# Performance work log

Hardware: AMD Instinct MI355X
Metric: run time of the kernel (lower is better)

## Reference

```python
import jax, jax.numpy as jnp
import numpy as np

N_NODES = 50000
N_EDGES = 800000
D_IN = 64
D_HID = 64
D_OUT = 64


def setup_inputs() -> dict:
    key = jax.random.key(0)
    ks = jax.random.split(key, 6)
    X = jax.random.normal(ks[0], (N_NODES, D_IN), dtype=jnp.float32)
    edge_index = jax.random.randint(ks[1], (2, N_EDGES), 0, N_NODES, dtype=jnp.int64)
    edge_weight = jax.random.uniform(ks[2], (N_EDGES,), dtype=jnp.float32)
    W1 = jax.random.normal(ks[3], (D_IN, D_HID), dtype=jnp.float32) / np.float32(np.sqrt(D_IN))
    b1 = jnp.zeros((D_HID,), dtype=jnp.float32)
    W2 = jax.random.normal(ks[4], (D_HID, D_OUT), dtype=jnp.float32) / np.float32(np.sqrt(D_HID))
    b2 = jnp.zeros((D_OUT,), dtype=jnp.float32)
    return {"X": X, "edge_weight": edge_weight, "W1": W1, "b1": b1,
            "W2": W2, "b2": b2, "edge_index": edge_index}


def reference(X, edge_weight, W1, b1, W2, b2, edge_index):
    # conv(A, X) = (A @ X) @ W + b with sparse A given as (edge_index, edge_weight)
    src = edge_index[0]
    dst = edge_index[1]

    def agg(H):
        # weighted neighborhood sum: [E, d] messages scattered to [N, d]
        msgs = edge_weight[:, None] * H[src]
        return jax.ops.segment_sum(msgs, dst, num_segments=N_NODES)

    # layer 1: conv -> relu (dropout p=0 is identity)
    H = jax.nn.relu(agg(X) @ W1 + b1)
    # last layer: conv, no final activation (l_act=None)
    return agg(H) @ W2 + b2
```

## Files before the change

### kernel.cpp

```cpp
#include <hip/hip_runtime.h>

#define D 64

#define NB 256
#define RB 256

template <bool PRE>
__global__ __launch_bounds__(256, 4) void gemm64_kernel(
    const float* __restrict__ A, const float* __restrict__ W,
    const float* __restrict__ bpre, float* __restrict__ out, int N) {
  __shared__ float sA[64][68];
  __shared__ float sW[64][68];
  const int t = threadIdx.x;
  const int rowBase = blockIdx.x * 64;

#pragma unroll
  for (int i = t * 4; i < 4096; i += 1024) {
    const int k = i >> 6, c = i & 63;
    *reinterpret_cast<float4*>(&sW[k][c]) =
        *reinterpret_cast<const float4*>(W + i);
  }
#pragma unroll
  for (int i = t * 4; i < 4096; i += 1024) {
    const int r = i >> 6, k = i & 63;
    const int row = rowBase + r;
    float4 a = make_float4(0.f, 0.f, 0.f, 0.f);
    if (row < N) a = *reinterpret_cast<const float4*>(A + (size_t)row * D + k);
    if (PRE) {
      const float4 b = *reinterpret_cast<const float4*>(bpre + k);
      a.x = fmaxf(a.x + b.x, 0.f);
      a.y = fmaxf(a.y + b.y, 0.f);
      a.z = fmaxf(a.z + b.z, 0.f);
      a.w = fmaxf(a.w + b.w, 0.f);
    }
    *reinterpret_cast<float4*>(&sA[r][k]) = a;
  }
  __syncthreads();

  const int ty = t >> 4, tx = t & 15;
  float4 acc0 = make_float4(0.f, 0.f, 0.f, 0.f);
  float4 acc1 = make_float4(0.f, 0.f, 0.f, 0.f);
  float4 acc2 = make_float4(0.f, 0.f, 0.f, 0.f);
  float4 acc3 = make_float4(0.f, 0.f, 0.f, 0.f);

#pragma unroll 4
  for (int kq = 0; kq < 16; ++kq) {
    const float4 w0 = *reinterpret_cast<const float4*>(&sW[kq * 4 + 0][tx * 4]);
    const float4 w1 = *reinterpret_cast<const float4*>(&sW[kq * 4 + 1][tx * 4]);
    const float4 w2 = *reinterpret_cast<const float4*>(&sW[kq * 4 + 2][tx * 4]);
    const float4 w3 = *reinterpret_cast<const float4*>(&sW[kq * 4 + 3][tx * 4]);
    const float4 a0 = *reinterpret_cast<const float4*>(&sA[ty * 4 + 0][kq * 4]);
    const float4 a1 = *reinterpret_cast<const float4*>(&sA[ty * 4 + 1][kq * 4]);
    const float4 a2 = *reinterpret_cast<const float4*>(&sA[ty * 4 + 2][kq * 4]);
    const float4 a3 = *reinterpret_cast<const float4*>(&sA[ty * 4 + 3][kq * 4]);
#define FMA4(ACC, AV)                                                     \
    ACC.x += AV.x * w0.x + AV.y * w1.x + AV.z * w2.x + AV.w * w3.x;       \
    ACC.y += AV.x * w0.y + AV.y * w1.y + AV.z * w2.y + AV.w * w3.y;       \
    ACC.z += AV.x * w0.z + AV.y * w1.z + AV.z * w2.z + AV.w * w3.z;       \
    ACC.w += AV.x * w0.w + AV.y * w1.w + AV.z * w2.w + AV.w * w3.w;
    FMA4(acc0, a0) FMA4(acc1, a1) FMA4(acc2, a2) FMA4(acc3, a3)
#undef FMA4
  }

  const int row0 = rowBase + ty * 4;
  if (row0 + 0 < N) *reinterpret_cast<float4*>(out + (size_t)(row0 + 0) * D + tx * 4) = acc0;
  if (row0 + 1 < N) *reinterpret_cast<float4*>(out + (size_t)(row0 + 1) * D + tx * 4) = acc1;
  if (row0 + 2 < N) *reinterpret_cast<float4*>(out + (size_t)(row0 + 2) * D + tx * 4) = acc2;
  if (row0 + 3 < N) *reinterpret_cast<float4*>(out + (size_t)(row0 + 3) * D + tx * 4) = acc3;
}

__global__ __launch_bounds__(256, 4) void hist_gemm_kernel(
    const int* __restrict__ dst, int* __restrict__ countsB, int E, int epb,
    const float* __restrict__ A, const float* __restrict__ W,
    float* __restrict__ out, int N) {
  __shared__ float sA[64][68];
  __shared__ float sW[64][68];
  const int t = threadIdx.x;

  if ((int)blockIdx.x < NB) {
    int* h = reinterpret_cast<int*>(&sA[0][0]);
    h[t] = 0;
    __syncthreads();
    const int base = blockIdx.x * epb;
    const int lim = min(base + epb, E);
    for (int i = base + t; i < lim; i += 256) atomicAdd(&h[dst[i] >> 8], 1);
    __syncthreads();
    countsB[blockIdx.x * RB + t] = h[t];
    return;
  }

  const int rowBase = ((int)blockIdx.x - NB) * 64;
#pragma unroll
  for (int i = t * 4; i < 4096; i += 1024) {
    const int k = i >> 6, c = i & 63;
    *reinterpret_cast<float4*>(&sW[k][c]) =
        *reinterpret_cast<const float4*>(W + i);
  }
#pragma unroll
  for (int i = t * 4; i < 4096; i += 1024) {
    const int r = i >> 6, k = i & 63;
    const int row = rowBase + r;
    float4 a = make_float4(0.f, 0.f, 0.f, 0.f);
    if (row < N) a = *reinterpret_cast<const float4*>(A + (size_t)row * D + k);
    *reinterpret_cast<float4*>(&sA[r][k]) = a;
  }
  __syncthreads();

  const int ty = t >> 4, tx = t & 15;
  float4 acc0 = make_float4(0.f, 0.f, 0.f, 0.f);
  float4 acc1 = make_float4(0.f, 0.f, 0.f, 0.f);
  float4 acc2 = make_float4(0.f, 0.f, 0.f, 0.f);
  float4 acc3 = make_float4(0.f, 0.f, 0.f, 0.f);

#pragma unroll 4
  for (int kq = 0; kq < 16; ++kq) {
    const float4 w0 = *reinterpret_cast<const float4*>(&sW[kq * 4 + 0][tx * 4]);
    const float4 w1 = *reinterpret_cast<const float4*>(&sW[kq * 4 + 1][tx * 4]);
    const float4 w2 = *reinterpret_cast<const float4*>(&sW[kq * 4 + 2][tx * 4]);
    const float4 w3 = *reinterpret_cast<const float4*>(&sW[kq * 4 + 3][tx * 4]);
    const float4 a0 = *reinterpret_cast<const float4*>(&sA[ty * 4 + 0][kq * 4]);
    const float4 a1 = *reinterpret_cast<const float4*>(&sA[ty * 4 + 1][kq * 4]);
    const float4 a2 = *reinterpret_cast<const float4*>(&sA[ty * 4 + 2][kq * 4]);
    const float4 a3 = *reinterpret_cast<const float4*>(&sA[ty * 4 + 3][kq * 4]);
#define FMA4(ACC, AV)                                                     \
    ACC.x += AV.x * w0.x + AV.y * w1.x + AV.z * w2.x + AV.w * w3.x;       \
    ACC.y += AV.x * w0.y + AV.y * w1.y + AV.z * w2.y + AV.w * w3.y;       \
    ACC.z += AV.x * w0.z + AV.y * w1.z + AV.z * w2.z + AV.w * w3.z;       \
    ACC.w += AV.x * w0.w + AV.y * w1.w + AV.z * w2.w + AV.w * w3.w;
    FMA4(acc0, a0) FMA4(acc1, a1) FMA4(acc2, a2) FMA4(acc3, a3)
#undef FMA4
  }

  const int row0 = rowBase + ty * 4;
  if (row0 + 0 < N) *reinterpret_cast<float4*>(out + (size_t)(row0 + 0) * D + tx * 4) = acc0;
  if (row0 + 1 < N) *reinterpret_cast<float4*>(out + (size_t)(row0 + 1) * D + tx * 4) = acc1;
  if (row0 + 2 < N) *reinterpret_cast<float4*>(out + (size_t)(row0 + 2) * D + tx * 4) = acc2;
  if (row0 + 3 < N) *reinterpret_cast<float4*>(out + (size_t)(row0 + 3) * D + tx * 4) = acc3;
}

__global__ __launch_bounds__(256) void p1_scatter_kernel(
    const int* __restrict__ src, const int* __restrict__ dst,
    const float* __restrict__ ew, const int* __restrict__ countsB,
    int* __restrict__ binBaseG, int2* __restrict__ tmp, int E, int epb) {
  __shared__ int s[RB];
  __shared__ int cur[RB];
  const int t = threadIdx.x;
  const int b = blockIdx.x;

  int total = 0, pre = 0;
#pragma unroll 8
  for (int i = 0; i < NB; ++i) {
    const int c = countsB[i * RB + t];
    if (i == b) pre = total;
    total += c;
  }
  s[t] = total;
  __syncthreads();
  for (int off = 1; off < 256; off <<= 1) {
    int x = (t >= off) ? s[t - off] : 0;
    __syncthreads();
    s[t] += x;
    __syncthreads();
  }
  const int binBase = s[t] - total;
  cur[t] = binBase + pre;
  if (b == 0) {
    binBaseG[t] = binBase;
    if (t == 255) binBaseG[256] = s[255];
  }
  __syncthreads();

  const int base = b * epb;
  const int lim = min(base + epb, E);
  for (int i = base + t; i < lim; i += 256) {
    const int d = dst[i];
    const unsigned sv = (unsigned)src[i];
    const float w = ew[i];
    const int pos = atomicAdd(&cur[d >> 8], 1);
    tmp[pos] = make_int2((int)((unsigned)d | (sv << 16)), __float_as_int(w));
  }
}

__global__ __launch_bounds__(256) void p2_kernel(
    const int2* __restrict__ tmp, const int* __restrict__ binBaseG,
    int* __restrict__ offs, int2* __restrict__ pairs, int N) {
  __shared__ int h[RB];
  __shared__ int s[RB];
  __shared__ int cur[RB];
  const int t = threadIdx.x;
  const int b = blockIdx.x;
  const int segBeg = binBaseG[b];
  const int segEnd = binBaseG[b + 1];

  h[t] = 0;
  __syncthreads();
  for (int i = segBeg + t; i < segEnd; i += 256)
    atomicAdd(&h[tmp[i].x & 255], 1);
  __syncthreads();

  const int v = h[t];
  s[t] = v;
  __syncthreads();
  for (int off = 1; off < 256; off <<= 1) {
    int x = (t >= off) ? s[t - off] : 0;
    __syncthreads();
    s[t] += x;
    __syncthreads();
  }
  const int excl = s[t] - v;
  cur[t] = segBeg + excl;
  const int node = b * RB + t;
  if (node <= N) offs[node] = segBeg + excl;
  __syncthreads();

  for (int i = segBeg + t; i < segEnd; i += 256) {
    const int2 r = tmp[i];
    const int lo = r.x & 255;
    const int pos = atomicAdd(&cur[lo], 1);
    pairs[pos] = make_int2((int)(((unsigned)r.x) >> 16), r.y);
  }
}

__global__ __launch_bounds__(256) void hist_kernel(
    const int* __restrict__ dst, int* __restrict__ deg,
    int* __restrict__ posw, int E) {
  int e = blockIdx.x * 256 + threadIdx.x;
  if (e < E) posw[e] = atomicAdd(&deg[dst[e]], 1);
}

#define SCAN_CHUNK 1024
__global__ __launch_bounds__(256) void scan_part_kernel(
    const int* __restrict__ deg, int* __restrict__ offs,
    int* __restrict__ bsums, int N) {
  __shared__ int s[256];
  const int t = threadIdx.x;
  const int base = blockIdx.x * SCAN_CHUNK + t * 4;
  int v0 = 0, v1 = 0, v2 = 0, v3 = 0;
  if (base + 3 < N) {
    const int4 v = *reinterpret_cast<const int4*>(deg + base);
    v0 = v.x; v1 = v.y; v2 = v.z; v3 = v.w;
  } else {
    if (base + 0 < N) v0 = deg[base + 0];
    if (base + 1 < N) v1 = deg[base + 1];
    if (base + 2 < N) v2 = deg[base + 2];
  }
  const int tsum = v0 + v1 + v2 + v3;
  s[t] = tsum;
  __syncthreads();
  for (int off = 1; off < 256; off <<= 1) {
    int x = (t >= off) ? s[t - off] : 0;
    __syncthreads();
    s[t] += x;
    __syncthreads();
  }
  const int excl = s[t] - tsum;
  if (base + 0 < N) offs[base + 0] = excl;
  if (base + 1 < N) offs[base + 1] = excl + v0;
  if (base + 2 < N) offs[base + 2] = excl + v0 + v1;
  if (base + 3 < N) offs[base + 3] = excl + v0 + v1 + v2;
  if (t == 255) bsums[blockIdx.x] = s[255];
}

__global__ __launch_bounds__(1024) void scan_sums_kernel(
    int* __restrict__ bsums, int* __restrict__ offsN, int nb) {
  __shared__ int s[1024];
  const int t = threadIdx.x;
  const int v = (t < nb) ? bsums[t] : 0;
  s[t] = v;
  __syncthreads();
  for (int off = 1; off < 1024; off <<= 1) {
    int x = (t >= off) ? s[t - off] : 0;
    __syncthreads();
    s[t] += x;
    __syncthreads();
  }
  if (t < nb) bsums[t] = s[t] - v;
  if (t == nb - 1) *offsN = s[t];
}

__global__ __launch_bounds__(256) void scan_add_kernel(
    int* __restrict__ offs, const int* __restrict__ bsums, int N) {
  const int i = blockIdx.x * 256 + threadIdx.x;
  if (i < N) offs[i] += bsums[i >> 10];
}

__global__ __launch_bounds__(256) void bucket_kernel(
    const int* __restrict__ src, const int* __restrict__ dst,
    const float* __restrict__ ew, const int* __restrict__ offs,
    const int* __restrict__ posw, int2* __restrict__ pairs, int E) {
  int e = blockIdx.x * 256 + threadIdx.x;
  if (e < E) {
    const int pos = offs[dst[e]] + posw[e];
    pairs[pos] = make_int2(src[e], __float_as_int(ew[e]));
  }
}

__global__ __launch_bounds__(256, 4) void agg_gemm_kernel(
    const float* __restrict__ H, const int* __restrict__ offs,
    const int2* __restrict__ pairs, const float* __restrict__ b1,
    const float* __restrict__ W, float* __restrict__ out, int N) {
  __shared__ float sA[64][68];
  __shared__ float sW[64][68];
  const int t = threadIdx.x;
  const int rowBase = blockIdx.x * 64;

#pragma unroll
  for (int i = t * 4; i < 4096; i += 1024) {
    const int k = i >> 6, c = i & 63;
    *reinterpret_cast<float4*>(&sW[k][c]) =
        *reinterpret_cast<const float4*>(W + i);
  }

  const int l4 = t & 15;
  const int sub = t >> 4;
  const float4 bb = *reinterpret_cast<const float4*>(b1 + l4 * 4);
#pragma unroll
  for (int p = 0; p < 4; ++p) {
    const int r = p * 16 + sub;
    const int node = rowBase + r;
    float4 A0 = make_float4(0.f, 0.f, 0.f, 0.f);
    float4 A1 = make_float4(0.f, 0.f, 0.f, 0.f);
    float4 A2 = make_float4(0.f, 0.f, 0.f, 0.f);
    float4 A3 = make_float4(0.f, 0.f, 0.f, 0.f);
    if (node < N) {
      const int beg = offs[node], end = offs[node + 1];
      int i = beg;
      for (; i + 4 <= end; i += 4) {
        const int2 p0 = pairs[i], p1 = pairs[i + 1], p2 = pairs[i + 2], p3 = pairs[i + 3];
        const float4 v0 = *reinterpret_cast<const float4*>(H + (size_t)p0.x * D + l4 * 4);
        const float4 v1 = *reinterpret_cast<const float4*>(H + (size_t)p1.x * D + l4 * 4);
        const float4 v2 = *reinterpret_cast<const float4*>(H + (size_t)p2.x * D + l4 * 4);
        const float4 v3 = *reinterpret_cast<const float4*>(H + (size_t)p3.x * D + l4 * 4);
        const float w0 = __int_as_float(p0.y), w1 = __int_as_float(p1.y);
        const float w2 = __int_as_float(p2.y), w3 = __int_as_float(p3.y);
        A0.x += w0 * v0.x; A0.y += w0 * v0.y; A0.z += w0 * v0.z; A0.w += w0 * v0.w;
        A1.x += w1 * v1.x; A1.y += w1 * v1.y; A1.z += w1 * v1.z; A1.w += w1 * v1.w;
        A2.x += w2 * v2.x; A2.y += w2 * v2.y; A2.z += w2 * v2.z; A2.w += w2 * v2.w;
        A3.x += w3 * v3.x; A3.y += w3 * v3.y; A3.z += w3 * v3.z; A3.w += w3 * v3.w;
      }
      for (; i < end; ++i) {
        const int2 pp = pairs[i];
        const float4 v = *reinterpret_cast<const float4*>(H + (size_t)pp.x * D + l4 * 4);
        const float w = __int_as_float(pp.y);
        A0.x += w * v.x; A0.y += w * v.y; A0.z += w * v.z; A0.w += w * v.w;
      }
    }
    float4 rr;
    rr.x = fmaxf((A0.x + A1.x) + (A2.x + A3.x) + bb.x, 0.f);
    rr.y = fmaxf((A0.y + A1.y) + (A2.y + A3.y) + bb.y, 0.f);
    rr.z = fmaxf((A0.z + A1.z) + (A2.z + A3.z) + bb.z, 0.f);
    rr.w = fmaxf((A0.w + A1.w) + (A2.w + A3.w) + bb.w, 0.f);
    *reinterpret_cast<float4*>(&sA[r][l4 * 4]) = rr;
  }
  __syncthreads();

  const int ty = t >> 4, tx = t & 15;
  float4 acc0 = make_float4(0.f, 0.f, 0.f, 0.f);
  float4 acc1 = make_float4(0.f, 0.f, 0.f, 0.f);
  float4 acc2 = make_float4(0.f, 0.f, 0.f, 0.f);
  float4 acc3 = make_float4(0.f, 0.f, 0.f, 0.f);

#pragma unroll 4
  for (int kq = 0; kq < 16; ++kq) {
    const float4 w0 = *reinterpret_cast<const float4*>(&sW[kq * 4 + 0][tx * 4]);
    const float4 w1 = *reinterpret_cast<const float4*>(&sW[kq * 4 + 1][tx * 4]);
    const float4 w2 = *reinterpret_cast<const float4*>(&sW[kq * 4 + 2][tx * 4]);
    const float4 w3 = *reinterpret_cast<const float4*>(&sW[kq * 4 + 3][tx * 4]);
    const float4 a0 = *reinterpret_cast<const float4*>(&sA[ty * 4 + 0][kq * 4]);
    const float4 a1 = *reinterpret_cast<const float4*>(&sA[ty * 4 + 1][kq * 4]);
    const float4 a2 = *reinterpret_cast<const float4*>(&sA[ty * 4 + 2][kq * 4]);
    const float4 a3 = *reinterpret_cast<const float4*>(&sA[ty * 4 + 3][kq * 4]);
#define FMA4(ACC, AV)                                                     \
    ACC.x += AV.x * w0.x + AV.y * w1.x + AV.z * w2.x + AV.w * w3.x;       \
    ACC.y += AV.x * w0.y + AV.y * w1.y + AV.z * w2.y + AV.w * w3.y;       \
    ACC.z += AV.x * w0.z + AV.y * w1.z + AV.z * w2.z + AV.w * w3.z;       \
    ACC.w += AV.x * w0.w + AV.y * w1.w + AV.z * w2.w + AV.w * w3.w;
    FMA4(acc0, a0) FMA4(acc1, a1) FMA4(acc2, a2) FMA4(acc3, a3)
#undef FMA4
  }

  const int row0 = rowBase + ty * 4;
  if (row0 + 0 < N) *reinterpret_cast<float4*>(out + (size_t)(row0 + 0) * D + tx * 4) = acc0;
  if (row0 + 1 < N) *reinterpret_cast<float4*>(out + (size_t)(row0 + 1) * D + tx * 4) = acc1;
  if (row0 + 2 < N) *reinterpret_cast<float4*>(out + (size_t)(row0 + 2) * D + tx * 4) = acc2;
  if (row0 + 3 < N) *reinterpret_cast<float4*>(out + (size_t)(row0 + 3) * D + tx * 4) = acc3;
}

template <bool BIAS>
__global__ __launch_bounds__(256) void gather_agg_kernel(
    const float* __restrict__ H, const int* __restrict__ offs,
    const int2* __restrict__ pairs,
    const float* __restrict__ bias, float* __restrict__ out, int N) {
  const int l4 = threadIdx.x & 15;
  const int node = blockIdx.x * 16 + (threadIdx.x >> 4);
  if (node >= N) return;
  const int beg = offs[node], end = offs[node + 1];
  float4 A0 = make_float4(0.f, 0.f, 0.f, 0.f);
  float4 A1 = make_float4(0.f, 0.f, 0.f, 0.f);
  float4 A2 = make_float4(0.f, 0.f, 0.f, 0.f);
  float4 A3 = make_float4(0.f, 0.f, 0.f, 0.f);
  int i = beg;
  for (; i + 4 <= end; i += 4) {
    const int2 p0 = pairs[i], p1 = pairs[i + 1], p2 = pairs[i + 2], p3 = pairs[i + 3];
    const float4 v0 = *reinterpret_cast<const float4*>(H + (size_t)p0.x * D + l4 * 4);
    const float4 v1 = *reinterpret_cast<const float4*>(H + (size_t)p1.x * D + l4 * 4);
    const float4 v2 = *reinterpret_cast<const float4*>(H + (size_t)p2.x * D + l4 * 4);
    const float4 v3 = *reinterpret_cast<const float4*>(H + (size_t)p3.x * D + l4 * 4);
    const float w0 = __int_as_float(p0.y), w1 = __int_as_float(p1.y);
    const float w2 = __int_as_float(p2.y), w3 = __int_as_float(p3.y);
    A0.x += w0 * v0.x; A0.y += w0 * v0.y; A0.z += w0 * v0.z; A0.w += w0 * v0.w;
    A1.x += w1 * v1.x; A1.y += w1 * v1.y; A1.z += w1 * v1.z; A1.w += w1 * v1.w;
    A2.x += w2 * v2.x; A2.y += w2 * v2.y; A2.z += w2 * v2.z; A2.w += w2 * v2.w;
    A3.x += w3 * v3.x; A3.y += w3 * v3.y; A3.z += w3 * v3.z; A3.w += w3 * v3.w;
  }
  for (; i < end; ++i) {
    const int2 p = pairs[i];
    const float4 v = *reinterpret_cast<const float4*>(H + (size_t)p.x * D + l4 * 4);
    const float w = __int_as_float(p.y);
    A0.x += w * v.x; A0.y += w * v.y; A0.z += w * v.z; A0.w += w * v.w;
  }
  float4 r;
  r.x = (A0.x + A1.x) + (A2.x + A3.x);
  r.y = (A0.y + A1.y) + (A2.y + A3.y);
  r.z = (A0.z + A1.z) + (A2.z + A3.z);
  r.w = (A0.w + A1.w) + (A2.w + A3.w);
  if (BIAS) {
    const float4 b = *reinterpret_cast<const float4*>(bias + l4 * 4);
    r.x += b.x; r.y += b.y; r.z += b.z; r.w += b.w;
  }
  *reinterpret_cast<float4*>(out + (size_t)node * D + l4 * 4) = r;
}

__global__ __launch_bounds__(256) void scatter_kernel(
    const float* __restrict__ H, const float* __restrict__ ew,
    const int* __restrict__ src, const int* __restrict__ dst,
    float* __restrict__ out, int nEdges) {
  const int tid = blockIdx.x * 256 + threadIdx.x;
  const int e = tid >> 4;
  if (e >= nEdges) return;
  const int c = (tid & 15) * 4;
  const float w = ew[e];
  const float4 v = *reinterpret_cast<const float4*>(H + (size_t)src[e] * D + c);
  float* o = out + (size_t)dst[e] * D + c;
  atomicAdd(o + 0, w * v.x);
  atomicAdd(o + 1, w * v.y);
  atomicAdd(o + 2, w * v.z);
  atomicAdd(o + 3, w * v.w);
}

__global__ __launch_bounds__(256) void fill_bias_kernel(
    float* __restrict__ out, const float* __restrict__ b, int total) {
  int i = blockIdx.x * 256 + threadIdx.x;
  if (i < total) out[i] = b[i & 63];
}

extern "C" void kernel_launch(void* const* d_in, const int* in_sizes, int n_in,
                              void* d_out, int out_size, void* d_ws,
                              size_t ws_size, hipStream_t stream) {
  const float* X  = (const float*)d_in[0];
  const float* ew = (const float*)d_in[1];
  const float* W1 = (const float*)d_in[2];
  const float* b1 = (const float*)d_in[3];
  const float* W2 = (const float*)d_in[4];
  const float* b2 = (const float*)d_in[5];
  const int*   ei = (const int*)d_in[6];

  const int N = in_sizes[0] / D;
  const int E = in_sizes[6] / 2;
  const int* src = ei;
  const int* dst = ei + E;
  float* out = (float*)d_out;

  char* ws = (char*)d_ws;
  float* buf0 = (float*)ws;                 ws += (size_t)N * D * 4;
  float* buf1 = (float*)ws;                 ws += (size_t)N * D * 4;
  const size_t baseBytes = (size_t)(ws - (char*)d_ws);
  int2*  pairs    = (int2*)ws;              ws += (size_t)E * 8;
  int*   offs     = (int*)ws;               ws += (size_t)(N + 1) * 4;
  int*   countsB  = (int*)ws;               ws += (size_t)NB * RB * 4;
  int*   binBaseG = (int*)ws;               ws += (size_t)(RB + 1) * 4;
  const size_t needBytes = (size_t)(ws - (char*)d_ws);

  const int gemmBlocks = (N + 63) / 64;
  const int aggBlocks  = (N + 15) / 16;
  const int edgeBlocks = (E + 255) / 256;

  if (ws_size >= needBytes) {
    if (N <= NB * RB && (size_t)N * D * 4 >= (size_t)E * 8) {
      int2* tmp = (int2*)buf1;
      const int epb = (E + NB - 1) / NB;
      hist_gemm_kernel<<<NB + gemmBlocks, 256, 0, stream>>>(
          dst, countsB, E, epb, X, W1, buf0, N);
      p1_scatter_kernel<<<NB, 256, 0, stream>>>(src, dst, ew, countsB,
                                                binBaseG, tmp, E, epb);
      p2_kernel<<<RB, 256, 0, stream>>>(tmp, binBaseG, offs, pairs, N);
    } else {
      int* deg   = (int*)buf0;
      int* bsums = (int*)buf0 + N;
      int* posw  = (int*)buf1;
      const int nb = (N + SCAN_CHUNK - 1) / SCAN_CHUNK;
      hipMemsetAsync(deg, 0, (size_t)N * 4, stream);
      hist_kernel<<<edgeBlocks, 256, 0, stream>>>(dst, deg, posw, E);
      scan_part_kernel<<<nb, 256, 0, stream>>>(deg, offs, bsums, N);
      scan_sums_kernel<<<1, 1024, 0, stream>>>(bsums, offs + N, nb);
      scan_add_kernel<<<(N + 255) / 256, 256, 0, stream>>>(offs, bsums, N);
      bucket_kernel<<<edgeBlocks, 256, 0, stream>>>(src, dst, ew, offs, posw, pairs, E);
      gemm64_kernel<false><<<gemmBlocks, 256, 0, stream>>>(X, W1, nullptr, buf0, N);
    }

    agg_gemm_kernel<<<gemmBlocks, 256, 0, stream>>>(buf0, offs, pairs, b1, W2, buf1, N);
    gather_agg_kernel<true><<<aggBlocks, 256, 0, stream>>>(buf1, offs, pairs, b2, out, N);
  } else if (ws_size >= baseBytes) {
    const int scatBlocks = (E * 16 + 255) / 256;
    const int fillBlocks = (N * D + 255) / 256;
    gemm64_kernel<false><<<gemmBlocks, 256, 0, stream>>>(X, W1, nullptr, buf0, N);
    hipMemsetAsync(buf1, 0, (size_t)N * D * 4, stream);
    scatter_kernel<<<scatBlocks, 256, 0, stream>>>(buf0, ew, src, dst, buf1, E);
    gemm64_kernel<true><<<gemmBlocks, 256, 0, stream>>>(buf1, W2, b1, buf0, N);
    fill_bias_kernel<<<fillBlocks, 256, 0, stream>>>(out, b2, N * D);
    scatter_kernel<<<scatBlocks, 256, 0, stream>>>(buf0, ew, src, dst, out, E);
  }
}
```

Measured before the change: 116.3 us.

## Use whole-wave per-node gathers and register-cached ranks in bucket sort pass

The aggregation kernels now give each node a full 64-lane wave: four groups of 16 lanes split that node's edges and are combined with xor shuffles, replacing the old scheme of one 16-lane group per node. This shortens the serial per-node edge loop and raises memory-level parallelism. The second sort pass now keeps records and their atomic ranks in registers, up to 20 per thread, and spills overflow ranks to a new global buffer, so it no longer re-reads tmp and runs a second atomic pass. The cost is more registers, shuffle work, and lanes left idle on low-degree nodes.

```diff
diff --git a/kernel.cpp b/kernel.cpp
--- a/kernel.cpp
+++ b/kernel.cpp
@@ -4,6 +4,52 @@
 
 #define NB 256
 #define RB 256
+#define P2CAP 20
+
+__device__ inline float4 f4zero() { return make_float4(0.f, 0.f, 0.f, 0.f); }
+
+__device__ inline float4 xor_add(float4 a, int m) {
+  a.x += __shfl_xor(a.x, m);
+  a.y += __shfl_xor(a.y, m);
+  a.z += __shfl_xor(a.z, m);
+  a.w += __shfl_xor(a.w, m);
+  return a;
+}
+
+__device__ inline float4 gather_rows(
+    const float* __restrict__ H, const int2* __restrict__ pairs,
+    int beg, int end, int g, int c4) {
+  float4 a0 = f4zero(), a1 = f4zero(), a2 = f4zero(), a3 = f4zero();
+  int i = beg + g;
+  for (; i + 12 < end; i += 16) {
+    const int2 p0 = pairs[i];
+    const int2 p1 = pairs[i + 4];
+    const int2 p2 = pairs[i + 8];
+    const int2 p3 = pairs[i + 12];
+    const float4 v0 = *reinterpret_cast<const float4*>(H + (size_t)p0.x * D + c4 * 4);
+    const float4 v1 = *reinterpret_cast<const float4*>(H + (size_t)p1.x * D + c4 * 4);
+    const float4 v2 = *reinterpret_cast<const float4*>(H + (size_t)p2.x * D + c4 * 4);
+    const float4 v3 = *reinterpret_cast<const float4*>(H + (size_t)p3.x * D + c4 * 4);
+    const float w0 = __int_as_float(p0.y), w1 = __int_as_float(p1.y);
+    const float w2 = __int_as_float(p2.y), w3 = __int_as_float(p3.y);
+    a0.x += w0 * v0.x; a0.y += w0 * v0.y; a0.z += w0 * v0.z; a0.w += w0 * v0.w;
+    a1.x += w1 * v1.x; a1.y += w1 * v1.y; a1.z += w1 * v1.z; a1.w += w1 * v1.w;
+    a2.x += w2 * v2.x; a2.y += w2 * v2.y; a2.z += w2 * v2.z; a2.w += w2 * v2.w;
+    a3.x += w3 * v3.x; a3.y += w3 * v3.y; a3.z += w3 * v3.z; a3.w += w3 * v3.w;
+  }
+  for (; i < end; i += 4) {
+    const int2 p = pairs[i];
+    const float4 v = *reinterpret_cast<const float4*>(H + (size_t)p.x * D + c4 * 4);
+    const float w = __int_as_float(p.y);
+    a0.x += w * v.x; a0.y += w * v.y; a0.z += w * v.z; a0.w += w * v.w;
+  }
+  float4 a;
+  a.x = (a0.x + a1.x) + (a2.x + a3.x);
+  a.y = (a0.y + a1.y) + (a2.y + a3.y);
+  a.z = (a0.z + a1.z) + (a2.z + a3.z);
+  a.w = (a0.w + a1.w) + (a2.w + a3.w);
+  return a;
+}
 
 template <bool PRE>
 __global__ __launch_bounds__(256, 4) void gemm64_kernel(
@@ -24,7 +70,7 @@
   for (int i = t * 4; i < 4096; i += 1024) {
     const int r = i >> 6, k = i & 63;
     const int row = rowBase + r;
-    float4 a = make_float4(0.f, 0.f, 0.f, 0.f);
+    float4 a = f4zero();
     if (row < N) a = *reinterpret_cast<const float4*>(A + (size_t)row * D + k);
     if (PRE) {
       const float4 b = *reinterpret_cast<const float4*>(bpre + k);
@@ -38,10 +84,7 @@
   __syncthreads();
 
   const int ty = t >> 4, tx = t & 15;
-  float4 acc0 = make_float4(0.f, 0.f, 0.f, 0.f);
-  float4 acc1 = make_float4(0.f, 0.f, 0.f, 0.f);
-  float4 acc2 = make_float4(0.f, 0.f, 0.f, 0.f);
-  float4 acc3 = make_float4(0.f, 0.f, 0.f, 0.f);
+  float4 acc0 = f4zero(), acc1 = f4zero(), acc2 = f4zero(), acc3 = f4zero();
 
 #pragma unroll 4
   for (int kq = 0; kq < 16; ++kq) {
@@ -100,17 +143,14 @@
   for (int i = t * 4; i < 4096; i += 1024) {
     const int r = i >> 6, k = i & 63;
     const int row = rowBase + r;
-    float4 a = make_float4(0.f, 0.f, 0.f, 0.f);
+    float4 a = f4zero();
     if (row < N) a = *reinterpret_cast<const float4*>(A + (size_t)row * D + k);
     *reinterpret_cast<float4*>(&sA[r][k]) = a;
   }
   __syncthreads();
 
   const int ty = t >> 4, tx = t & 15;
-  float4 acc0 = make_float4(0.f, 0.f, 0.f, 0.f);
-  float4 acc1 = make_float4(0.f, 0.f, 0.f, 0.f);
-  float4 acc2 = make_float4(0.f, 0.f, 0.f, 0.f);
-  float4 acc3 = make_float4(0.f, 0.f, 0.f, 0.f);
+  float4 acc0 = f4zero(), acc1 = f4zero(), acc2 = f4zero(), acc3 = f4zero();
 
 #pragma unroll 4
   for (int kq = 0; kq < 16; ++kq) {
@@ -183,19 +223,33 @@
 
 __global__ __launch_bounds__(256) void p2_kernel(
     const int2* __restrict__ tmp, const int* __restrict__ binBaseG,
+    int* __restrict__ rankG,
     int* __restrict__ offs, int2* __restrict__ pairs, int N) {
   __shared__ int h[RB];
   __shared__ int s[RB];
-  __shared__ int cur[RB];
   const int t = threadIdx.x;
   const int b = blockIdx.x;
   const int segBeg = binBaseG[b];
   const int segEnd = binBaseG[b + 1];
+  const int segLen = segEnd - segBeg;
 
   h[t] = 0;
   __syncthreads();
-  for (int i = segBeg + t; i < segEnd; i += 256)
-    atomicAdd(&h[tmp[i].x & 255], 1);
+
+  const int cnt = (segLen - t + 255) >> 8;
+  int2 rec[P2CAP];
+  int  rk[P2CAP];
+#pragma unroll
+  for (int k = 0; k < P2CAP; ++k) {
+    if (k < cnt) {
+      const int i = segBeg + t + (k << 8);
+      const int2 r = tmp[i];
+      rec[k] = r;
+      rk[k] = atomicAdd(&h[r.x & 255], 1);
+    }
+  }
+  for (int i = segBeg + (P2CAP << 8) + t; i < segEnd; i += 256)
+    rankG[i] = atomicAdd(&h[tmp[i].x & 255], 1);
   __syncthreads();
 
   const int v = h[t];
@@ -208,16 +262,24 @@
     __syncthreads();
   }
   const int excl = s[t] - v;
-  cur[t] = segBeg + excl;
   const int node = b * RB + t;
   if (node <= N) offs[node] = segBeg + excl;
   __syncthreads();
-
-  for (int i = segBeg + t; i < segEnd; i += 256) {
+  h[t] = segBeg + excl;
+  __syncthreads();
+
+#pragma unroll
+  for (int k = 0; k < P2CAP; ++k) {
+    if (k < cnt) {
+      const int2 r = rec[k];
+      pairs[h[r.x & 255] + rk[k]] =
+          make_int2((int)(((unsigned)r.x) >> 16), r.y);
+    }
+  }
+  for (int i = segBeg + (P2CAP << 8) + t; i < segEnd; i += 256) {
     const int2 r = tmp[i];
-    const int lo = r.x & 255;
-    const int pos = atomicAdd(&cur[lo], 1);
-    pairs[pos] = make_int2((int)(((unsigned)r.x) >> 16), r.y);
+    pairs[h[r.x & 255] + rankG[i]] =
+        make_int2((int)(((unsigned)r.x) >> 16), r.y);
   }
 }
 
@@ -311,54 +373,35 @@
         *reinterpret_cast<const float4*>(W + i);
   }
 
-  const int l4 = t & 15;
-  const int sub = t >> 4;
-  const float4 bb = *reinterpret_cast<const float4*>(b1 + l4 * 4);
-#pragma unroll
-  for (int p = 0; p < 4; ++p) {
-    const int r = p * 16 + sub;
+  const int wv = t >> 6;
+  const int lane = t & 63;
+  const int g = lane >> 4;
+  const int c4 = lane & 15;
+  const float4 bb = *reinterpret_cast<const float4*>(b1 + c4 * 4);
+
+  for (int sidx = 0; sidx < 16; ++sidx) {
+    const int r = wv * 16 + sidx;
     const int node = rowBase + r;
-    float4 A0 = make_float4(0.f, 0.f, 0.f, 0.f);
-    float4 A1 = make_float4(0.f, 0.f, 0.f, 0.f);
-    float4 A2 = make_float4(0.f, 0.f, 0.f, 0.f);
-    float4 A3 = make_float4(0.f, 0.f, 0.f, 0.f);
+    float4 a = f4zero();
     if (node < N) {
       const int beg = offs[node], end = offs[node + 1];
-      int i = beg;
-      for (; i + 4 <= end; i += 4) {
-        const int2 p0 = pairs[i], p1 = pairs[i + 1], p2 = pairs[i + 2], p3 = pairs[i + 3];
-        const float4 v0 = *reinterpret_cast<const float4*>(H + (size_t)p0.x * D + l4 * 4);
-        const float4 v1 = *reinterpret_cast<const float4*>(H + (size_t)p1.x * D + l4 * 4);
-        const float4 v2 = *reinterpret_cast<const float4*>(H + (size_t)p2.x * D + l4 * 4);
-        const float4 v3 = *reinterpret_cast<const float4*>(H + (size_t)p3.x * D + l4 * 4);
-        const float w0 = __int_as_float(p0.y), w1 = __int_as_float(p1.y);
-        const float w2 = __int_as_float(p2.y), w3 = __int_as_float(p3.y);
-        A0.x += w0 * v0.x; A0.y += w0 * v0.y; A0.z += w0 * v0.z; A0.w += w0 * v0.w;
-        A1.x += w1 * v1.x; A1.y += w1 * v1.y; A1.z += w1 * v1.z; A1.w += w1 * v1.w;
-        A2.x += w2 * v2.x; A2.y += w2 * v2.y; A2.z += w2 * v2.z; A2.w += w2 * v2.w;
-        A3.x += w3 * v3.x; A3.y += w3 * v3.y; A3.z += w3 * v3.z; A3.w += w3 * v3.w;
-      }
-      for (; i < end; ++i) {
-        const int2 pp = pairs[i];
-        const float4 v = *reinterpret_cast<const float4*>(H + (size_t)pp.x * D + l4 * 4);
-        const float w = __int_as_float(pp.y);
-        A0.x += w * v.x; A0.y += w * v.y; A0.z += w * v.z; A0.w += w * v.w;
-      }
-    }
-    float4 rr;
-    rr.x = fmaxf((A0.x + A1.x) + (A2.x + A3.x) + bb.x, 0.f);
-    rr.y = fmaxf((A0.y + A1.y) + (A2.y + A3.y) + bb.y, 0.f);
-    rr.z = fmaxf((A0.z + A1.z) + (A2.z + A3.z) + bb.z, 0.f);
-    rr.w = fmaxf((A0.w + A1.w) + (A2.w + A3.w) + bb.w, 0.f);
-    *reinterpret_cast<float4*>(&sA[r][l4 * 4]) = rr;
+      a = gather_rows(H, pairs, beg, end, g, c4);
+    }
+    a = xor_add(a, 16);
+    a = xor_add(a, 32);
+    if (g == 0) {
+      float4 rr;
+      rr.x = fmaxf(a.x + bb.x, 0.f);
+      rr.y = fmaxf(a.y + bb.y, 0.f);
+      rr.z = fmaxf(a.z + bb.z, 0.f);
+      rr.w = fmaxf(a.w + bb.w, 0.f);
+      *reinterpret_cast<float4*>(&sA[r][c4 * 4]) = rr;
+    }
   }
   __syncthreads();
 
   const int ty = t >> 4, tx = t & 15;
-  float4 acc0 = make_float4(0.f, 0.f, 0.f, 0.f);
-  float4 acc1 = make_float4(0.f, 0.f, 0.f, 0.f);
-  float4 acc2 = make_float4(0.f, 0.f, 0.f, 0.f);
-  float4 acc3 = make_float4(0.f, 0.f, 0.f, 0.f);
+  float4 acc0 = f4zero(), acc1 = f4zero(), acc2 = f4zero(), acc3 = f4zero();
 
 #pragma unroll 4
   for (int kq = 0; kq < 16; ++kq) {
@@ -387,48 +430,26 @@
 }
 
 template <bool BIAS>
-__global__ __launch_bounds__(256) void gather_agg_kernel(
+__global__ __launch_bounds__(256) void wave_agg_kernel(
     const float* __restrict__ H, const int* __restrict__ offs,
-    const int2* __restrict__ pairs,
-    const float* __restrict__ bias, float* __restrict__ out, int N) {
-  const int l4 = threadIdx.x & 15;
-  const int node = blockIdx.x * 16 + (threadIdx.x >> 4);
+    const int2* __restrict__ pairs, const float* __restrict__ bias,
+    float* __restrict__ out, int N) {
+  const int lane = threadIdx.x & 63;
+  const int g = lane >> 4;
+  const int c4 = lane & 15;
+  const int node = blockIdx.x * 4 + (threadIdx.x >> 6);
   if (node >= N) return;
   const int beg = offs[node], end = offs[node + 1];
-  float4 A0 = make_float4(0.f, 0.f, 0.f, 0.f);
-  float4 A1 = make_float4(0.f, 0.f, 0.f, 0.f);
-  float4 A2 = make_float4(0.f, 0.f, 0.f, 0.f);
-  float4 A3 = make_float4(0.f, 0.f, 0.f, 0.f);
-  int i = beg;
-  for (; i + 4 <= end; i += 4) {
-    const int2 p0 = pairs[i], p1 = pairs[i + 1], p2 = pairs[i + 2], p3 = pairs[i + 3];
-    const float4 v0 = *reinterpret_cast<const float4*>(H + (size_t)p0.x * D + l4 * 4);
-    const float4 v1 = *reinterpret_cast<const float4*>(H + (size_t)p1.x * D + l4 * 4);
-    const float4 v2 = *reinterpret_cast<const float4*>(H + (size_t)p2.x * D + l4 * 4);
-    const float4 v3 = *reinterpret_cast<const float4*>(H + (size_t)p3.x * D + l4 * 4);
-    const float w0 = __int_as_float(p0.y), w1 = __int_as_float(p1.y);
-    const float w2 = __int_as_float(p2.y), w3 = __int_as_float(p3.y);
-    A0.x += w0 * v0.x; A0.y += w0 * v0.y; A0.z += w0 * v0.z; A0.w += w0 * v0.w;
-    A1.x += w1 * v1.x; A1.y += w1 * v1.y; A1.z += w1 * v1.z; A1.w += w1 * v1.w;
-    A2.x += w2 * v2.x; A2.y += w2 * v2.y; A2.z += w2 * v2.z; A2.w += w2 * v2.w;
-    A3.x += w3 * v3.x; A3.y += w3 * v3.y; A3.z += w3 * v3.z; A3.w += w3 * v3.w;
-  }
-  for (; i < end; ++i) {
-    const int2 p = pairs[i];
-    const float4 v = *reinterpret_cast<const float4*>(H + (size_t)p.x * D + l4 * 4);
-    const float w = __int_as_float(p.y);
-    A0.x += w * v.x; A0.y += w * v.y; A0.z += w * v.z; A0.w += w * v.w;
-  }
-  float4 r;
-  r.x = (A0.x + A1.x) + (A2.x + A3.x);
-  r.y = (A0.y + A1.y) + (A2.y + A3.y);
-  r.z = (A0.z + A1.z) + (A2.z + A3.z);
-  r.w = (A0.w + A1.w) + (A2.w + A3.w);
-  if (BIAS) {
-    const float4 b = *reinterpret_cast<const float4*>(bias + l4 * 4);
-    r.x += b.x; r.y += b.y; r.z += b.z; r.w += b.w;
-  }
-  *reinterpret_cast<float4*>(out + (size_t)node * D + l4 * 4) = r;
+  float4 a = gather_rows(H, pairs, beg, end, g, c4);
+  a = xor_add(a, 16);
+  a = xor_add(a, 32);
+  if (g == 0) {
+    if (BIAS) {
+      const float4 b = *reinterpret_cast<const float4*>(bias + c4 * 4);
+      a.x += b.x; a.y += b.y; a.z += b.z; a.w += b.w;
+    }
+    *reinterpret_cast<float4*>(out + (size_t)node * D + c4 * 4) = a;
+  }
 }
 
 __global__ __launch_bounds__(256) void scatter_kernel(
@@ -479,10 +500,11 @@
   int*   offs     = (int*)ws;               ws += (size_t)(N + 1) * 4;
   int*   countsB  = (int*)ws;               ws += (size_t)NB * RB * 4;
   int*   binBaseG = (int*)ws;               ws += (size_t)(RB + 1) * 4;
+  int*   rankG    = (int*)ws;               ws += (size_t)E * 4;
   const size_t needBytes = (size_t)(ws - (char*)d_ws);
 
   const int gemmBlocks = (N + 63) / 64;
-  const int aggBlocks  = (N + 15) / 16;
+  const int waveBlocks = (N + 3) / 4;
   const int edgeBlocks = (E + 255) / 256;
 
   if (ws_size >= needBytes) {
@@ -493,7 +515,7 @@
           dst, countsB, E, epb, X, W1, buf0, N);
       p1_scatter_kernel<<<NB, 256, 0, stream>>>(src, dst, ew, countsB,
                                                 binBaseG, tmp, E, epb);
-      p2_kernel<<<RB, 256, 0, stream>>>(tmp, binBaseG, offs, pairs, N);
+      p2_kernel<<<RB, 256, 0, stream>>>(tmp, binBaseG, rankG, offs, pairs, N);
     } else {
       int* deg   = (int*)buf0;
       int* bsums = (int*)buf0 + N;
@@ -509,7 +531,7 @@
     }
 
     agg_gemm_kernel<<<gemmBlocks, 256, 0, stream>>>(buf0, offs, pairs, b1, W2, buf1, N);
-    gather_agg_kernel<true><<<aggBlocks, 256, 0, stream>>>(buf1, offs, pairs, b2, out, N);
+    wave_agg_kernel<true><<<waveBlocks, 256, 0, stream>>>(buf1, offs, pairs, b2, out, N);
   } else if (ws_size >= baseBytes) {
     const int scatBlocks = (E * 16 + 255) / 256;
     const int fillBlocks = (N * D + 255) / 256;
```

New measurement: 130.9 us. 1.13x slower.
